# Kernel tuning notes

Measured on AMD Instinct MI355X. Metric: run time of the kernel, lower is better.

## Reference

```python
import jax, jax.numpy as jnp
import numpy as np

HID = 2048
NH = 16
HD = HID // NH
FF = 8192
SEQ = 2048
B = 1
EPS = 1e-05
ROPE_BASE = 10000.0


def _layernorm(x, w, b):
    mu = jnp.mean(x, axis=-1, keepdims=True)
    var = jnp.mean(jnp.square(x - mu), axis=-1, keepdims=True)
    return (x - mu) * jax.lax.rsqrt(var + EPS) * w + b


def _rope(x, offset):
    # x: [B, S, H, D]; rotate-half LLaMA-style rotary embedding
    S, D = x.shape[1], x.shape[3]
    inv_freq = 1.0 / (ROPE_BASE ** (jnp.arange(0, D, 2, dtype=jnp.float32) / D))  # [D/2]
    pos = jnp.arange(S, dtype=jnp.float32) + offset
    ang = pos[:, None] * inv_freq[None, :]                     # [S, D/2]
    cos = jnp.cos(ang)[None, :, None, :]                       # [1,S,1,D/2]
    sin = jnp.sin(ang)[None, :, None, :]
    x1, x2 = x[..., : D // 2], x[..., D // 2 :]
    return jnp.concatenate([x1 * cos - x2 * sin, x2 * cos + x1 * sin], axis=-1)


def setup_inputs() -> dict:
    key = jax.random.key(0)
    ks = jax.random.split(key, 16)
    sd = 0.02
    inp = {
        "hidden_states": jax.random.normal(ks[0], (B, SEQ, HID), dtype=jnp.float32),
        # additive causal mask as fed to multi_head_attention_forward
        "attention_mask": jnp.where(
            jnp.tril(jnp.ones((SEQ, SEQ), dtype=bool)), 0.0, -1e9
        ).astype(jnp.float32),
        "ln1_w": jnp.ones((HID,), jnp.float32),
        "ln1_b": jnp.zeros((HID,), jnp.float32),
        "ln2_w": jnp.ones((HID,), jnp.float32),
        "ln2_b": jnp.zeros((HID,), jnp.float32),
        "wq": jax.random.normal(ks[1], (HID, HID), jnp.float32) * sd,
        "bq": jnp.zeros((HID,), jnp.float32),
        "wk": jax.random.normal(ks[2], (HID, HID), jnp.float32) * sd,
        "bk": jnp.zeros((HID,), jnp.float32),
        "wv": jax.random.normal(ks[3], (HID, HID), jnp.float32) * sd,
        "bv": jnp.zeros((HID,), jnp.float32),
        "wo": jax.random.normal(ks[4], (HID, HID), jnp.float32) * sd,
        "bo": jnp.zeros((HID,), jnp.float32),
        "w_gate": jax.random.normal(ks[5], (FF, HID), jnp.float32) * sd,
        "w_up": jax.random.normal(ks[6], (FF, HID), jnp.float32) * sd,
        "w_down": jax.random.normal(ks[7], (HID, FF), jnp.float32) * sd,
        "total_seq_len": SEQ,
    }
    return inp


def reference(hidden_states, attention_mask, ln1_w, ln1_b, ln2_w, ln2_b,
              wq, bq, wk, bk, wv, bv, wo, bo, w_gate, w_up, w_down,
              total_seq_len):
    Bv, S, _ = hidden_states.shape
    x = _layernorm(hidden_states, ln1_w, ln1_b)
    q = (x @ wq.T + bq).reshape(Bv, S, NH, HD)
    k = (x @ wk.T + bk).reshape(Bv, S, NH, HD)
    v = (x @ wv.T + bv).reshape(Bv, S, NH, HD)
    offset = total_seq_len - S  # 0 for prefill
    q = _rope(q, offset)
    k = _rope(k, offset)
    # cache of max_sequence_length zeros concatenated with k/v then sliced to the
    # last total_seq_len entries == just the current k/v when total_seq_len == S
    scale = 1.0 / np.sqrt(HD)
    scores = jnp.einsum("bshd,bthd->bhst", q, k) * scale + attention_mask[None, None]
    probs = jax.nn.softmax(scores, axis=-1)
    attn = jnp.einsum("bhst,bthd->bshd", probs, v).reshape(Bv, S, HID)
    attn = attn @ wo.T + bo
    h = hidden_states + attn
    y = _layernorm(h, ln2_w, ln2_b)
    ffn = (jax.nn.silu(y @ w_gate.T) * (y @ w_up.T)) @ w_down.T
    return h + ffn
```

## Files before the change

### kernel.cpp

```cpp
#include <hip/hip_runtime.h>

#define HIDN 2048
#define NHEAD 16
#define HDIM 128
#define FFDIM 8192
#define SEQLEN 2048

typedef __attribute__((ext_vector_type(8))) __bf16 bf16x8;
typedef __attribute__((ext_vector_type(4))) float f32x4;
typedef __attribute__((ext_vector_type(4))) unsigned short u16x4;
typedef __attribute__((ext_vector_type(8))) unsigned short u16x8;

__device__ __forceinline__ unsigned short f2bfu(float f) {
    unsigned int u = __float_as_uint(f);
    unsigned int r = u + 0x7fffu + ((u >> 16) & 1u);
    return (unsigned short)(r >> 16);
}
__device__ __forceinline__ float bfu2f(unsigned short u) {
    return __uint_as_float(((unsigned int)u) << 16);
}

__device__ __forceinline__ void gload16(const void* g, void* l) {
    __builtin_amdgcn_global_load_lds(
        (const __attribute__((address_space(1))) unsigned int*)g,
        (__attribute__((address_space(3))) unsigned int*)l,
        16, 0, 0);
}

__global__ __launch_bounds__(256)
void conv_f32_bf16(const float* __restrict__ src, unsigned short* __restrict__ dst) {
    int i = blockIdx.x * 256 + threadIdx.x;
    float4 a = ((const float4*)src)[i * 2];
    float4 b = ((const float4*)src)[i * 2 + 1];
    u16x8 v;
    v[0] = f2bfu(a.x); v[1] = f2bfu(a.y); v[2] = f2bfu(a.z); v[3] = f2bfu(a.w);
    v[4] = f2bfu(b.x); v[5] = f2bfu(b.y); v[6] = f2bfu(b.z); v[7] = f2bfu(b.w);
    *(u16x8*)(dst + (size_t)i * 8) = v;
}

__global__ __launch_bounds__(256)
void conv3_f32_bf16(const float* __restrict__ s0, const float* __restrict__ s1,
                    const float* __restrict__ s2, unsigned short* __restrict__ dst) {
    int i = blockIdx.x * 256 + threadIdx.x;
    int m = i >> 19;
    int li = i & ((1 << 19) - 1);
    const float* s = (m == 0) ? s0 : (m == 1) ? s1 : s2;
    float4 a = ((const float4*)s)[li * 2];
    float4 b = ((const float4*)s)[li * 2 + 1];
    u16x8 v;
    v[0] = f2bfu(a.x); v[1] = f2bfu(a.y); v[2] = f2bfu(a.z); v[3] = f2bfu(a.w);
    v[4] = f2bfu(b.x); v[5] = f2bfu(b.y); v[6] = f2bfu(b.z); v[7] = f2bfu(b.w);
    *(u16x8*)(dst + (size_t)i * 8) = v;
}

__global__ __launch_bounds__(256)
void ln_bf16(const float* __restrict__ x, const float* __restrict__ w,
             const float* __restrict__ b, unsigned short* __restrict__ out) {
    const int row = blockIdx.x;
    const int tid = threadIdx.x;
    const float* xr = x + (size_t)row * HIDN;
    float4 v0 = ((const float4*)xr)[tid];
    float4 v1 = ((const float4*)xr)[tid + 256];
    float s = v0.x + v0.y + v0.z + v0.w + v1.x + v1.y + v1.z + v1.w;
    float q = v0.x*v0.x + v0.y*v0.y + v0.z*v0.z + v0.w*v0.w
            + v1.x*v1.x + v1.y*v1.y + v1.z*v1.z + v1.w*v1.w;
    for (int o = 32; o > 0; o >>= 1) {
        s += __shfl_down(s, o, 64);
        q += __shfl_down(q, o, 64);
    }
    __shared__ float red[8];
    const int wid = tid >> 6;
    if ((tid & 63) == 0) { red[wid] = s; red[4 + wid] = q; }
    __syncthreads();
    float st = red[0] + red[1] + red[2] + red[3];
    float qt = red[4] + red[5] + red[6] + red[7];
    float mu = st * (1.0f / HIDN);
    float var = qt * (1.0f / HIDN) - mu * mu;
    float rs = rsqrtf(var + 1e-5f);
    unsigned short* orow = out + (size_t)row * HIDN;
    int i0 = tid * 4, i1 = (tid + 256) * 4;
    orow[i0 + 0] = f2bfu((v0.x - mu) * rs * w[i0 + 0] + b[i0 + 0]);
    orow[i0 + 1] = f2bfu((v0.y - mu) * rs * w[i0 + 1] + b[i0 + 1]);
    orow[i0 + 2] = f2bfu((v0.z - mu) * rs * w[i0 + 2] + b[i0 + 2]);
    orow[i0 + 3] = f2bfu((v0.w - mu) * rs * w[i0 + 3] + b[i0 + 3]);
    orow[i1 + 0] = f2bfu((v1.x - mu) * rs * w[i1 + 0] + b[i1 + 0]);
    orow[i1 + 1] = f2bfu((v1.y - mu) * rs * w[i1 + 1] + b[i1 + 1]);
    orow[i1 + 2] = f2bfu((v1.z - mu) * rs * w[i1 + 2] + b[i1 + 2]);
    orow[i1 + 3] = f2bfu((v1.w - mu) * rs * w[i1 + 3] + b[i1 + 3]);
}

__global__ __launch_bounds__(256)
void rope_kernel(unsigned short* __restrict__ qk, const int* __restrict__ tsl) {
    int id = blockIdx.x * 256 + threadIdx.x;
    int p  = id & 63;
    int hh = (id >> 6) & 31;
    int s  = id >> 11;
    int off = tsl[0] - SEQLEN;
    float inv = exp2f((float)p * -0.20762050593f);
    float ang = (float)(s + off) * inv;
    float c, sn;
    __sincosf(ang, &sn, &c);
    size_t base = (size_t)s * 4096 + hh * 128 + p;
    float x1 = bfu2f(qk[base]);
    float x2 = bfu2f(qk[base + 64]);
    qk[base]      = f2bfu(x1 * c - x2 * sn);
    qk[base + 64] = f2bfu(x2 * c + x1 * sn);
}

#define BAR __builtin_amdgcn_s_barrier()
#define VM4 asm volatile("s_waitcnt vmcnt(4)" ::: "memory")
#define VM0 asm volatile("s_waitcnt vmcnt(0)" ::: "memory")

#define STAGE_A(tile, h) { const int k0_ = k_start + (tile) * 64;                      \
  _Pragma("unroll") for (int i_ = 0; i_ < 2; ++i_) {                                   \
    int d_ = (h) * 16384 + i_ * 8192 + tid * 16;                                       \
    int r_ = d_ >> 7;                                                                  \
    int cb_ = (d_ & 127) ^ ((r_ & 7) << 4);                                            \
    gload16((const char*)Ab + ((size_t)(brow + r_) * lda + k0_) * 2 + cb_,             \
            smem + ((tile) & 1) * 65536 + (h) * 16384 + i_ * 8192 + w * 1024); } }

#define STAGE_B(tile, h) { const int k0_ = k_start + (tile) * 64;                      \
  _Pragma("unroll") for (int i_ = 0; i_ < 2; ++i_) {                                   \
    int d_ = (h) * 16384 + i_ * 8192 + tid * 16;                                       \
    int r_ = d_ >> 7;                                                                  \
    int cb_ = (d_ & 127) ^ ((r_ & 7) << 4);                                            \
    gload16((const char*)Bb + ((size_t)(bcol + r_) * ldb + k0_) * 2 + cb_,             \
            smem + ((tile) & 1) * 65536 + 32768 + (h) * 16384 + i_ * 8192 + w * 1024); } }

#define LDB(BO)                                                                        \
  _Pragma("unroll") for (int n_ = 0; n_ < 4; ++n_)                                     \
  _Pragma("unroll") for (int kk_ = 0; kk_ < 2; ++kk_)                                  \
    bF[n_][kk_] = *(const bf16x8*)(smem + (BO) + bbase + n_ * 2048 + colb[kk_]);

#define LDA2(BO, MP)                                                                   \
  _Pragma("unroll") for (int dm_ = 0; dm_ < 2; ++dm_)                                  \
  _Pragma("unroll") for (int kk_ = 0; kk_ < 2; ++kk_)                                  \
    aF[dm_][kk_] = *(const bf16x8*)(smem + (BO) + abase + ((MP) * 2 + dm_) * 2048 + colb[kk_]);

#define MM(MP)                                                                         \
  __builtin_amdgcn_s_setprio(1);                                                       \
  _Pragma("unroll") for (int dm_ = 0; dm_ < 2; ++dm_)                                  \
  _Pragma("unroll") for (int n_ = 0; n_ < 4; ++n_)                                     \
  _Pragma("unroll") for (int kk_ = 0; kk_ < 2; ++kk_)                                  \
    acc[(MP) * 2 + dm_][n_] = __builtin_amdgcn_mfma_f32_16x16x32_bf16(                 \
        aF[dm_][kk_], bF[n_][kk_], acc[(MP) * 2 + dm_][n_], 0, 0, 0);                  \
  __builtin_amdgcn_s_setprio(0);

template<int EPI>
__global__ __launch_bounds__(512, 1)
void gemm256(const unsigned short* __restrict__ Ab, int lda,
             const unsigned short* __restrict__ Bb, int ldb,
             int k_len, int nbx, int ldc,
             const float* __restrict__ bias0, const float* __restrict__ bias1,
             const float* __restrict__ bias2,
             unsigned short* __restrict__ outB, unsigned short* __restrict__ outV) {
    extern __shared__ char smem[];
    const int tid = threadIdx.x;
    const int w = tid >> 6, lane = tid & 63;
    const int lr = lane & 15, lg = lane >> 4;
    const int wrow = (w >> 2) * 128;
    const int wc = w & 3;

    const int cpx = nbx >> 3;
    const int xcd = blockIdx.x & 7;
    const int loc = blockIdx.x >> 3;
    const int bx = xcd * cpx + loc % cpx;
    const int by = loc / cpx;
    const int brow = by * 256, bcol = bx * 256;
    const int k_start = blockIdx.y * k_len;

    const int xorv = (lr & 7) << 4;
    int colb[2];
    colb[0] = (lg * 16) ^ xorv;
    colb[1] = (64 + lg * 16) ^ xorv;
    const int abase = (wrow + lr) * 128;
    const int bbase = 32768 + (wc * 64 + lr) * 128;

    f32x4 acc[8][4];
#pragma unroll
    for (int m = 0; m < 8; ++m)
#pragma unroll
        for (int n = 0; n < 4; ++n) acc[m][n] = (f32x4){0.f, 0.f, 0.f, 0.f};

    bf16x8 bF[4][2], aF[2][2];

    const int NT = k_len >> 6;
    const int NIT = NT >> 1;

    STAGE_A(0, 0); STAGE_A(0, 1); STAGE_B(0, 0); STAGE_B(0, 1);
    STAGE_B(1, 0); STAGE_B(1, 1);
    VM4; BAR;

    for (int it = 0; it < NIT; ++it) {
        const int T = 2 * it;
        const bool s2 = (T + 2) < NT, s3 = (T + 3) < NT;
        LDB(0); LDA2(0, 0); STAGE_A(T + 1, 0); MM(0); BAR;
        LDA2(0, 1); STAGE_A(T + 1, 1); MM(1); BAR;
        LDA2(0, 2); if (s2) STAGE_B(T + 2, 0); MM(2); BAR;
        LDA2(0, 3); if (s2) STAGE_B(T + 2, 1); MM(3);
        if (s2) { VM4; } else { VM0; }
        BAR;
        LDB(65536); LDA2(65536, 0); if (s2) STAGE_A(T + 2, 0); MM(0); BAR;
        LDA2(65536, 1); if (s2) STAGE_A(T + 2, 1); MM(1); BAR;
        LDA2(65536, 2); if (s3) STAGE_B(T + 3, 0); MM(2); BAR;
        LDA2(65536, 3); if (s3) STAGE_B(T + 3, 1); MM(3);
        if (s3) { VM4; } else { VM0; }
        BAR;
    }

    char* sw = smem + w * 16384;
    const bool vblk = (EPI == 0) && (bcol >= 4096);

    if (!vblk) {
#pragma unroll
        for (int n = 0; n < 4; ++n) {
            const int col = bcol + wc * 64 + n * 16 + lr;
            float bv = 0.f;
            if (EPI == 0) bv = (col < 2048) ? bias0[col] : bias1[col - 2048];
#pragma unroll
            for (int m = 0; m < 8; ++m)
#pragma unroll
                for (int j = 0; j < 4; ++j) {
                    const int r = m * 16 + lg * 4 + j;
                    const int cb = ((n * 16 + lr) * 2) ^ ((r & 7) << 4);
                    *(unsigned short*)(sw + r * 128 + cb) = f2bfu(acc[m][n][j] + bv);
                }
        }
        const int rl = lane >> 3, cl = lane & 7;
#pragma unroll
        for (int it2 = 0; it2 < 16; ++it2) {
            const int r = it2 * 8 + rl;
            const int cb = (cl * 16) ^ ((r & 7) << 4);
            u16x8 val = *(const u16x8*)(sw + r * 128 + cb);
            const int gr = brow + wrow + r;
            const int gcol = bcol + wc * 64 + cl * 8;
            if (EPI == 0) {
                *(u16x8*)(outB + (size_t)gr * 4096 + gcol) = val;
            } else if (EPI == 1) {
                *(u16x8*)(outB + (size_t)gr * ldc + gcol) = val;
            } else if (EPI == 3) {
                unsigned short* gp = outB + (size_t)gr * ldc + gcol;
                u16x8 gv = *(const u16x8*)gp;
                u16x8 ov;
#pragma unroll
                for (int e = 0; e < 8; ++e) {
                    float g = bfu2f(gv[e]);
                    float uu = bfu2f(val[e]);
                    ov[e] = f2bfu(g / (1.0f + __expf(-g)) * uu);
                }
                *(u16x8*)gp = ov;
            } else {
                *(u16x8*)(outB + (size_t)blockIdx.y * 4194304 + (size_t)gr * ldc + gcol) = val;
            }
        }
    } else {
#pragma unroll
        for (int n = 0; n < 4; ++n) {
            const int c = n * 16 + lr;
            const float bv = bias2[bcol - 4096 + wc * 64 + c];
            const int cx = (c & 7) << 4;
#pragma unroll
            for (int m = 0; m < 8; ++m) {
                const int r0 = m * 16 + lg * 4;
                u16x4 pk;
#pragma unroll
                for (int j = 0; j < 4; ++j) pk[j] = f2bfu(acc[m][n][j] + bv);
                *(u16x4*)(sw + c * 256 + ((r0 * 2) ^ cx)) = pk;
            }
        }
        const int cg = lane >> 4, rl2 = lane & 15;
#pragma unroll
        for (int it2 = 0; it2 < 16; ++it2) {
            const int c = it2 * 4 + cg;
            const int rb = (rl2 * 16) ^ ((c & 7) << 4);
            u16x8 val = *(const u16x8*)(sw + c * 256 + rb);
            const int d = bcol - 4096 + wc * 64 + c;
            *(u16x8*)(outV + (size_t)d * SEQLEN + brow + wrow + rl2 * 8) = val;
        }
    }
}

__global__ __launch_bounds__(256)
void reduce4_add(const unsigned short* __restrict__ part, float* __restrict__ out) {
    int i = blockIdx.x * 256 + threadIdx.x;
    float4 o = ((const float4*)out)[i];
#pragma unroll
    for (int sk = 0; sk < 4; ++sk) {
        u16x4 p = ((const u16x4*)(part + (size_t)sk * 4194304))[i];
        o.x += bfu2f(p[0]); o.y += bfu2f(p[1]); o.z += bfu2f(p[2]); o.w += bfu2f(p[3]);
    }
    ((float4*)out)[i] = o;
}

__global__ __launch_bounds__(256)
void reduce4_wo(const unsigned short* __restrict__ part, const float* __restrict__ h,
                const float* __restrict__ bias, float* __restrict__ out) {
    int i = blockIdx.x * 256 + threadIdx.x;
    float4 o = ((const float4*)h)[i];
    int col = (i & 511) * 4;
    o.x += bias[col]; o.y += bias[col + 1]; o.z += bias[col + 2]; o.w += bias[col + 3];
#pragma unroll
    for (int sk = 0; sk < 4; ++sk) {
        u16x4 p = ((const u16x4*)(part + (size_t)sk * 4194304))[i];
        o.x += bfu2f(p[0]); o.y += bfu2f(p[1]); o.z += bfu2f(p[2]); o.w += bfu2f(p[3]);
    }
    ((float4*)out)[i] = o;
}

#define PST 72
__global__ __launch_bounds__(256)
void attn_kernel(const unsigned short* __restrict__ QK, const unsigned short* __restrict__ VT,
                 unsigned short* __restrict__ O) {
    __shared__ __align__(16) unsigned short Ks[2][64 * 128];
    __shared__ __align__(16) unsigned short Vs[2][128 * 64];
    __shared__ __align__(16) unsigned short Ps[4][16 * PST];
    const int tid = threadIdx.x;
    const int lane = tid & 63;
    const int w = tid >> 6;
    const int lr = lane & 15, lg = lane >> 4;

    const int id = blockIdx.x;
    const int pair = id & 7;
    const int j0 = id >> 3;
    const int h = pair * 2 + (j0 & 1);
    const int qb = 31 - (j0 >> 1);
    const int q0 = qb * 64;
    const int qw = q0 + w * 16;

    const unsigned short* Qb = QK + (size_t)qw * 4096 + h * 128;
    const unsigned short* Kb = QK + 2048 + h * 128;
    const unsigned short* Vb = VT + (size_t)(h * 128) * SEQLEN;

    bf16x8 qa[4];
#pragma unroll
    for (int c = 0; c < 4; ++c)
        qa[c] = *(const bf16x8*)(Qb + (size_t)lr * 4096 + c * 32 + lg * 8);

    int krow[4], kcb[4], vrow[4], vcb[4];
#pragma unroll
    for (int ch = 0; ch < 4; ++ch) {
        int d = ch * 4096 + w * 1024 + lane * 16;
        krow[ch] = d >> 8;
        kcb[ch]  = (d & 255) ^ ((krow[ch] & 7) << 4);
        vrow[ch] = d >> 7;
        vcb[ch]  = (d & 127) ^ ((vrow[ch] & 7) << 4);
    }

    f32x4 acc[8];
#pragma unroll
    for (int dt = 0; dt < 8; ++dt) acc[dt] = (f32x4){0.f, 0.f, 0.f, 0.f};
    float mrow[4] = {-INFINITY, -INFINITY, -INFINITY, -INFINITY};
    float lrow[4] = {0.f, 0.f, 0.f, 0.f};

    const float sc = 0.08838834764831845f;
    const int ntile = qb + 1;

#pragma unroll
    for (int ch = 0; ch < 4; ++ch) {
        gload16(Kb + (size_t)krow[ch] * 4096 + (kcb[ch] >> 1),
                (char*)&Ks[0][0] + ch * 4096 + w * 1024);
        gload16(Vb + (size_t)vrow[ch] * SEQLEN + (vcb[ch] >> 1),
                (char*)&Vs[0][0] + ch * 4096 + w * 1024);
    }
    __syncthreads();

    for (int tt = 0; tt < ntile; ++tt) {
        const int cur = tt & 1;
        const int t0 = tt * 64;
        if (tt + 1 < ntile) {
            const int t1 = t0 + 64;
#pragma unroll
            for (int ch = 0; ch < 4; ++ch) {
                gload16(Kb + (size_t)(t1 + krow[ch]) * 4096 + (kcb[ch] >> 1),
                        (char*)&Ks[cur ^ 1][0] + ch * 4096 + w * 1024);
                gload16(Vb + (size_t)vrow[ch] * SEQLEN + t1 + (vcb[ch] >> 1),
                        (char*)&Vs[cur ^ 1][0] + ch * 4096 + w * 1024);
            }
        }
        f32x4 s[4];
#pragma unroll
        for (int th = 0; th < 4; ++th) s[th] = (f32x4){0.f, 0.f, 0.f, 0.f};
        __builtin_amdgcn_s_setprio(1);
#pragma unroll
        for (int th = 0; th < 4; ++th) {
            const int row = th * 16 + lr;
#pragma unroll
            for (int c = 0; c < 4; ++c) {
                bf16x8 kb = *(const bf16x8*)((char*)&Ks[cur][0] + row * 256 +
                                             ((c * 64 + lg * 16) ^ ((lr & 7) << 4)));
                s[th] = __builtin_amdgcn_mfma_f32_16x16x32_bf16(qa[c], kb, s[th], 0, 0, 0);
            }
        }
        __builtin_amdgcn_s_setprio(0);
#pragma unroll
        for (int th = 0; th < 4; ++th) {
            int tg = t0 + th * 16 + lr;
#pragma unroll
            for (int jj = 0; jj < 4; ++jj) {
                int qg = qw + lg * 4 + jj;
                s[th][jj] = s[th][jj] * sc + (tg <= qg ? 0.f : -1e9f);
            }
        }
        float mt[4];
#pragma unroll
        for (int jj = 0; jj < 4; ++jj)
            mt[jj] = fmaxf(fmaxf(s[0][jj], s[1][jj]), fmaxf(s[2][jj], s[3][jj]));
#pragma unroll
        for (int o = 8; o > 0; o >>= 1)
#pragma unroll
            for (int jj = 0; jj < 4; ++jj) mt[jj] = fmaxf(mt[jj], __shfl_xor(mt[jj], o, 16));
        bool need = false;
#pragma unroll
        for (int jj = 0; jj < 4; ++jj) need = need || (mt[jj] > mrow[jj] + 4.0f);
        if (__any(need)) {
#pragma unroll
            for (int jj = 0; jj < 4; ++jj) {
                float mn = fmaxf(mrow[jj], mt[jj]);
                float a = __expf(mrow[jj] - mn);
                mrow[jj] = mn;
                lrow[jj] *= a;
#pragma unroll
                for (int dt = 0; dt < 8; ++dt) acc[dt][jj] *= a;
            }
        }
        float ps[4] = {0.f, 0.f, 0.f, 0.f};
#pragma unroll
        for (int th = 0; th < 4; ++th)
#pragma unroll
            for (int jj = 0; jj < 4; ++jj) {
                float p = __expf(s[th][jj] - mrow[jj]);
                s[th][jj] = p;
                ps[jj] += p;
            }
#pragma unroll
        for (int o = 8; o > 0; o >>= 1)
#pragma unroll
            for (int jj = 0; jj < 4; ++jj) ps[jj] += __shfl_xor(ps[jj], o, 16);
#pragma unroll
        for (int jj = 0; jj < 4; ++jj) lrow[jj] += ps[jj];
#pragma unroll
        for (int th = 0; th < 4; ++th)
#pragma unroll
            for (int jj = 0; jj < 4; ++jj)
                Ps[w][(lg * 4 + jj) * PST + th * 16 + lr] = f2bfu(s[th][jj]);
        bf16x8 pa[2];
#pragma unroll
        for (int ks = 0; ks < 2; ++ks)
            pa[ks] = *(const bf16x8*)&Ps[w][lr * PST + ks * 32 + lg * 8];
        __builtin_amdgcn_s_setprio(1);
#pragma unroll
        for (int dt = 0; dt < 8; ++dt) {
            const int d = dt * 16 + lr;
#pragma unroll
            for (int ks = 0; ks < 2; ++ks) {
                bf16x8 vb = *(const bf16x8*)((char*)&Vs[cur][0] + d * 128 +
                                             ((ks * 64 + lg * 16) ^ ((lr & 7) << 4)));
                acc[dt] = __builtin_amdgcn_mfma_f32_16x16x32_bf16(pa[ks], vb, acc[dt], 0, 0, 0);
            }
        }
        __builtin_amdgcn_s_setprio(0);
        __syncthreads();
    }
    float invl[4];
#pragma unroll
    for (int jj = 0; jj < 4; ++jj) invl[jj] = 1.0f / lrow[jj];
#pragma unroll
    for (int dt = 0; dt < 8; ++dt)
#pragma unroll
        for (int jj = 0; jj < 4; ++jj)
            O[(size_t)(qw + lg * 4 + jj) * HIDN + h * HDIM + dt * 16 + lr] = f2bfu(acc[dt][jj] * invl[jj]);
}

extern "C" void kernel_launch(void* const* d_in, const int* in_sizes, int n_in,
                              void* d_out, int out_size, void* d_ws, size_t ws_size,
                              hipStream_t stream) {
    const float* hidden = (const float*)d_in[0];
    const float* ln1w = (const float*)d_in[2];
    const float* ln1b = (const float*)d_in[3];
    const float* ln2w = (const float*)d_in[4];
    const float* ln2b = (const float*)d_in[5];
    const float* wq = (const float*)d_in[6];
    const float* bq = (const float*)d_in[7];
    const float* wk = (const float*)d_in[8];
    const float* bk = (const float*)d_in[9];
    const float* wv = (const float*)d_in[10];
    const float* bv = (const float*)d_in[11];
    const float* wo = (const float*)d_in[12];
    const float* bo = (const float*)d_in[13];
    const float* wg = (const float*)d_in[14];
    const float* wu = (const float*)d_in[15];
    const float* wd = (const float*)d_in[16];
    const int* tsl = (const int*)d_in[17];
    float* out = (float*)d_out;

    char* ws = (char*)d_ws;
    const size_t MB = 1024 * 1024;
    unsigned short* Wbuf = (unsigned short*)(ws);
    unsigned short* qk   = (unsigned short*)(ws + 32 * MB);
    unsigned short* vt   = (unsigned short*)(ws + 48 * MB);
    unsigned short* x_bf = (unsigned short*)(ws + 56 * MB);
    unsigned short* g_bf = (unsigned short*)(ws + 64 * MB);
    unsigned short* part = qk;
    unsigned short* y_bf = vt;

    const int HID2 = HIDN * HIDN;
    const int CONV_HID = HID2 / 8 / 256;
    const int CONV_FF  = FFDIM * HIDN / 8 / 256;
    const size_t LDSZ = 131072;

    conv3_f32_bf16<<<3 * CONV_HID, 256, 0, stream>>>(wq, wk, wv, Wbuf);
    ln_bf16<<<SEQLEN, 256, 0, stream>>>(hidden, ln1w, ln1b, x_bf);
    gemm256<0><<<dim3(192, 1), 512, LDSZ, stream>>>(x_bf, HIDN, Wbuf, HIDN, HIDN, 24, 0,
                                                    bq, bk, bv, qk, vt);
    rope_kernel<<<SEQLEN * 32 * 64 / 256, 256, 0, stream>>>(qk, tsl);
    attn_kernel<<<512, 256, 0, stream>>>(qk, vt, x_bf);

    conv_f32_bf16<<<CONV_HID, 256, 0, stream>>>(wo, Wbuf);
    gemm256<4><<<dim3(64, 4), 512, LDSZ, stream>>>(x_bf, HIDN, Wbuf, HIDN, 512, 8, HIDN,
                                                   nullptr, nullptr, nullptr, g_bf, nullptr);
    reduce4_wo<<<4096, 256, 0, stream>>>(g_bf, hidden, bo, out);

    ln_bf16<<<SEQLEN, 256, 0, stream>>>(out, ln2w, ln2b, y_bf);
    conv_f32_bf16<<<CONV_FF, 256, 0, stream>>>(wg, Wbuf);
    gemm256<1><<<dim3(256, 1), 512, LDSZ, stream>>>(y_bf, HIDN, Wbuf, HIDN, HIDN, 32, FFDIM,
                                                    nullptr, nullptr, nullptr, g_bf, nullptr);
    conv_f32_bf16<<<CONV_FF, 256, 0, stream>>>(wu, Wbuf);
    gemm256<3><<<dim3(256, 1), 512, LDSZ, stream>>>(y_bf, HIDN, Wbuf, HIDN, HIDN, 32, FFDIM,
                                                    nullptr, nullptr, nullptr, g_bf, nullptr);
    conv_f32_bf16<<<CONV_FF, 256, 0, stream>>>(wd, Wbuf);
    gemm256<4><<<dim3(64, 4), 512, LDSZ, stream>>>(g_bf, FFDIM, Wbuf, FFDIM, 2048, 8, HIDN,
                                                   nullptr, nullptr, nullptr, part, nullptr);
    reduce4_add<<<4096, 256, 0, stream>>>(part, out);
}
```

Before: 450.7 us.

## Double-buffer A fragments in registers and drop intra-tile barriers in GEMM loop

The GEMM main loop now keeps two register sets for A fragments. Each set's LDS reads are issued while the MFMAs on the other set run, with explicit lgkmcnt waits and sched_barriers to hold that order. The barriers per 64-wide K tile drop from four to two, and the first fragment loads for the next tile are moved to the end of the previous iteration. This aims to hide LDS read latency and cut synchronisation stalls, at the cost of extra VGPRs and a redundant trailing LDS read on the last iteration.

```diff
diff --git a/kernel.cpp b/kernel.cpp
--- a/kernel.cpp
+++ b/kernel.cpp
@@ -110,6 +110,10 @@
 #define BAR __builtin_amdgcn_s_barrier()
 #define VM4 asm volatile("s_waitcnt vmcnt(4)" ::: "memory")
 #define VM0 asm volatile("s_waitcnt vmcnt(0)" ::: "memory")
+#define LGK4 do { asm volatile("s_waitcnt lgkmcnt(4)" ::: "memory"); \
+                  __builtin_amdgcn_sched_barrier(0); } while (0)
+#define LGK0 do { asm volatile("s_waitcnt lgkmcnt(0)" ::: "memory"); \
+                  __builtin_amdgcn_sched_barrier(0); } while (0)
 
 #define STAGE_A(tile, h) { const int k0_ = k_start + (tile) * 64;                      \
   _Pragma("unroll") for (int i_ = 0; i_ < 2; ++i_) {                                   \
@@ -132,18 +136,18 @@
   _Pragma("unroll") for (int kk_ = 0; kk_ < 2; ++kk_)                                  \
     bF[n_][kk_] = *(const bf16x8*)(smem + (BO) + bbase + n_ * 2048 + colb[kk_]);
 
-#define LDA2(BO, MP)                                                                   \
+#define LDA_SET(BO, MP, SET)                                                           \
   _Pragma("unroll") for (int dm_ = 0; dm_ < 2; ++dm_)                                  \
   _Pragma("unroll") for (int kk_ = 0; kk_ < 2; ++kk_)                                  \
-    aF[dm_][kk_] = *(const bf16x8*)(smem + (BO) + abase + ((MP) * 2 + dm_) * 2048 + colb[kk_]);
-
-#define MM(MP)                                                                         \
+    SET[dm_][kk_] = *(const bf16x8*)(smem + (BO) + abase + ((MP) * 2 + dm_) * 2048 + colb[kk_]);
+
+#define MM_SET(SET, MP)                                                                \
   __builtin_amdgcn_s_setprio(1);                                                       \
   _Pragma("unroll") for (int dm_ = 0; dm_ < 2; ++dm_)                                  \
   _Pragma("unroll") for (int n_ = 0; n_ < 4; ++n_)                                     \
   _Pragma("unroll") for (int kk_ = 0; kk_ < 2; ++kk_)                                  \
     acc[(MP) * 2 + dm_][n_] = __builtin_amdgcn_mfma_f32_16x16x32_bf16(                 \
-        aF[dm_][kk_], bF[n_][kk_], acc[(MP) * 2 + dm_][n_], 0, 0, 0);                  \
+        SET[dm_][kk_], bF[n_][kk_], acc[(MP) * 2 + dm_][n_], 0, 0, 0);                 \
   __builtin_amdgcn_s_setprio(0);
 
 template<int EPI>
@@ -182,7 +186,7 @@
 #pragma unroll
         for (int n = 0; n < 4; ++n) acc[m][n] = (f32x4){0.f, 0.f, 0.f, 0.f};
 
-    bf16x8 bF[4][2], aF[2][2];
+    bf16x8 bF[4][2], aFa[2][2], aFb[2][2];
 
     const int NT = k_len >> 6;
     const int NIT = NT >> 1;
@@ -190,22 +194,33 @@
     STAGE_A(0, 0); STAGE_A(0, 1); STAGE_B(0, 0); STAGE_B(0, 1);
     STAGE_B(1, 0); STAGE_B(1, 1);
     VM4; BAR;
+    LDB(0); LDA_SET(0, 0, aFa);
 
     for (int it = 0; it < NIT; ++it) {
         const int T = 2 * it;
         const bool s2 = (T + 2) < NT, s3 = (T + 3) < NT;
-        LDB(0); LDA2(0, 0); STAGE_A(T + 1, 0); MM(0); BAR;
-        LDA2(0, 1); STAGE_A(T + 1, 1); MM(1); BAR;
-        LDA2(0, 2); if (s2) STAGE_B(T + 2, 0); MM(2); BAR;
-        LDA2(0, 3); if (s2) STAGE_B(T + 2, 1); MM(3);
+        STAGE_A(T + 1, 0); LDA_SET(0, 1, aFb); LGK4; MM_SET(aFa, 0);
+        STAGE_A(T + 1, 1); LDA_SET(0, 2, aFa); LGK4; MM_SET(aFb, 1);
+        BAR;
+        if (s2) STAGE_B(T + 2, 0);
+        LDA_SET(0, 3, aFb); LGK4; MM_SET(aFa, 2);
+        if (s2) STAGE_B(T + 2, 1);
+        LGK0; MM_SET(aFb, 3);
         if (s2) { VM4; } else { VM0; }
         BAR;
-        LDB(65536); LDA2(65536, 0); if (s2) STAGE_A(T + 2, 0); MM(0); BAR;
-        LDA2(65536, 1); if (s2) STAGE_A(T + 2, 1); MM(1); BAR;
-        LDA2(65536, 2); if (s3) STAGE_B(T + 3, 0); MM(2); BAR;
-        LDA2(65536, 3); if (s3) STAGE_B(T + 3, 1); MM(3);
+        LDB(65536); LDA_SET(65536, 0, aFa);
+        if (s2) STAGE_A(T + 2, 0);
+        LDA_SET(65536, 1, aFb); LGK4; MM_SET(aFa, 0);
+        if (s2) STAGE_A(T + 2, 1);
+        LDA_SET(65536, 2, aFa); LGK4; MM_SET(aFb, 1);
+        BAR;
+        if (s3) STAGE_B(T + 3, 0);
+        LDA_SET(65536, 3, aFb); LGK4; MM_SET(aFa, 2);
+        if (s3) STAGE_B(T + 3, 1);
+        LGK0; MM_SET(aFb, 3);
         if (s3) { VM4; } else { VM0; }
         BAR;
+        LDB(0); LDA_SET(0, 0, aFa);
     }
 
     char* sw = smem + w * 16384;
```

Result: no change. 449.6 us (-0.2%).
